# Optimization experiments

Measured on AMD Instinct MI355X. Metric: run time of the kernel, lower is better.

## Reference

```python
import jax, jax.numpy as jnp
import numpy as np

EPS = 1e-3  # kernel epsilon used in Performer generalized kernel
B, H, N, D, M = 1, 8, 1024, 64, 128  # batch, heads, seq, dim_heads, nb_features


def _gaussian_orthogonal_matrix(m, d, seed=0):
    # GaussianOrthogonalRandomMatrix with scaling=0: stacked QR blocks, rows
    # rescaled by chi-distributed norms of gaussian d-vectors.
    rng = np.random.default_rng(seed)
    blocks = []
    for _ in range(m // d):
        g = rng.standard_normal((d, d))
        qmat, _ = np.linalg.qr(g)
        blocks.append(qmat.T)
    proj = np.concatenate(blocks, axis=0)  # [m, d], orthonormal rows per block
    mult = np.linalg.norm(rng.standard_normal((m, d)), axis=1)  # chi norms
    return (mult[:, None] * proj).astype(np.float32)


def setup_inputs() -> dict:
    key = jax.random.key(0)
    kq, kk, kv = jax.random.split(key, 3)
    q = jax.random.normal(kq, (B, H, N, D), dtype=jnp.float32)
    k = jax.random.normal(kk, (B, H, N, D), dtype=jnp.float32)
    v = jax.random.normal(kv, (B, H, N, D), dtype=jnp.float32)
    proj = jnp.asarray(_gaussian_orthogonal_matrix(M, D))
    return {"q": q, "k": k, "v": v, "proj": proj}


def _generalized_kernel(x, proj):
    # kernel_fn(relu)( (x / d**0.25) @ proj^T ) + eps
    normalizer = 1.0 / (x.shape[-1] ** 0.25)
    xp = jnp.einsum('bhnd,md->bhnm', x * normalizer, proj)
    return jax.nn.relu(xp) + EPS


def reference(q, k, v, proj):
    qp = _generalized_kernel(q, proj)  # [B,H,N,M]
    kp = _generalized_kernel(k, proj)  # [B,H,N,M]
    # causal linear attention
    k_cumsum = jnp.cumsum(kp, axis=-2)                              # [B,H,N,M]
    context = jnp.einsum('bhnm,bhne->bhnme', kp, v)                 # [B,H,N,M,D]
    context = jnp.cumsum(context, axis=-3)                          # prefix sums over n
    context = context / k_cumsum[..., None]                         # normalize
    out = jnp.einsum('bhnme,bhnm->bhne', context, qp)               # [B,H,N,D]
    return out
```

## Files before the change

kernel.cpp:

```cpp
#include <hip/hip_runtime.h>

static constexpr int H = 8, N = 1024, D = 64, M = 128, CHUNK = 128, NC = 8;
static constexpr float EPS = 1e-3f;
static constexpr float NORM = 0.35355339059327373f;

typedef __attribute__((ext_vector_type(8))) short short8;
typedef __attribute__((ext_vector_type(4))) float f32x4;

__device__ inline unsigned short f2bf(float x) {
    unsigned u = __float_as_uint(x);
    return (unsigned short)((u + 0x7fffu + ((u >> 16) & 1u)) >> 16);
}
__device__ inline float bf2f(unsigned short u) {
    return __uint_as_float(((unsigned)u) << 16);
}
__device__ inline ushort4 pack4(float4 g) {
    return (ushort4){f2bf(g.x), f2bf(g.y), f2bf(g.z), f2bf(g.w)};
}

__global__ __launch_bounds__(512) void k_projg(const float* __restrict__ q,
                                               const float* __restrict__ k,
                                               const float* __restrict__ proj,
                                               const float* __restrict__ v,
                                               unsigned short* __restrict__ qpb,
                                               unsigned short* __restrict__ kpb,
                                               unsigned short* __restrict__ Gpb,
                                               float* __restrict__ kpart) {
    __shared__ __align__(16) short smem[30208];
    short* projb = smem;
    short* xb = smem + 9216;
    short* obuf = smem + 13824;
    short* kpT = smem + 22528;
    short* vT = smem + 27648;
    const int tid = threadIdx.x;
    const int rblk = blockIdx.x;
    const int h = blockIdx.y;
    const int rowbase = h * N + rblk * 32;
    const int lane = tid & 63, wv = tid >> 6;
    const int rt = wv & 3, mh = wv >> 2;
    const int fr = lane & 15, fq = lane >> 4;

    for (int i4 = tid; i4 < 2048; i4 += 512) {
        int m = i4 >> 4, dq = i4 & 15;
        *(ushort4*)&projb[m * 72 + dq * 4] = pack4(*(const float4*)&proj[i4 * 4]);
    }
    {
        int r = tid >> 4, dq = tid & 15;
        float4 g = *(const float4*)&q[(rowbase + r) * D + dq * 4];
        g.x *= NORM; g.y *= NORM; g.z *= NORM; g.w *= NORM;
        *(ushort4*)&xb[r * 72 + dq * 4] = pack4(g);
        float4 gk = *(const float4*)&k[(rowbase + r) * D + dq * 4];
        gk.x *= NORM; gk.y *= NORM; gk.z *= NORM; gk.w *= NORM;
        *(ushort4*)&xb[(32 + r) * 72 + dq * 4] = pack4(gk);
        int rv = tid & 31, e4 = (tid >> 5) * 4;
        float4 gv = *(const float4*)&v[(rowbase + rv) * D + e4];
        vT[(e4 + 0) * 40 + rv] = (short)f2bf(gv.x);
        vT[(e4 + 1) * 40 + rv] = (short)f2bf(gv.y);
        vT[(e4 + 2) * 40 + rv] = (short)f2bf(gv.z);
        vT[(e4 + 3) * 40 + rv] = (short)f2bf(gv.w);
    }
    __syncthreads();

    f32x4 accp[4];
#pragma unroll
    for (int i = 0; i < 4; i++) accp[i] = (f32x4){0.f, 0.f, 0.f, 0.f};
#pragma unroll
    for (int kt = 0; kt < 2; kt++) {
        short8 a = *(const short8*)&xb[(16 * rt + fr) * 72 + kt * 32 + fq * 8];
#pragma unroll
        for (int i = 0; i < 4; i++) {
            const int mt = mh * 4 + i;
            short8 bb = *(const short8*)&projb[(16 * mt + fr) * 72 + kt * 32 + fq * 8];
            accp[i] = __builtin_amdgcn_mfma_f32_16x16x32_bf16(a, bb, accp[i], 0, 0, 0);
        }
    }
#pragma unroll
    for (int i = 0; i < 4; i++) {
        const int mt = mh * 4 + i;
#pragma unroll
        for (int reg = 0; reg < 4; reg++) {
            const int r = 16 * rt + fq * 4 + reg;
            const int m = 16 * mt + fr;
            unsigned short bv = f2bf(fmaxf(accp[i][reg], 0.f) + EPS);
            obuf[r * 136 + m] = (short)bv;
            if (rt >= 2) kpT[m * 40 + (r - 32)] = (short)bv;
        }
    }
    __syncthreads();

    for (int i = tid; i < 2048; i += 512) {
        int r = i >> 5, cu = i & 31;
        ushort4 val = *(const ushort4*)&obuf[r * 136 + cu * 4];
        unsigned short* g = (r < 32) ? &qpb[(rowbase + r) * M + cu * 4]
                                     : &kpb[(rowbase + r - 32) * M + cu * 4];
        *(ushort4*)g = val;
    }
    const int gb = h * 32 + rblk;
    if (tid < 128) {
        float ks = 0.f;
#pragma unroll 8
        for (int r = 0; r < 32; r++) ks += bf2f((unsigned short)kpT[tid * 40 + r]);
        kpart[gb * M + tid] = ks;
    }
    __syncthreads();

    f32x4 gacc[4];
#pragma unroll
    for (int et = 0; et < 4; et++) gacc[et] = (f32x4){0.f, 0.f, 0.f, 0.f};
    {
        short8 a = *(const short8*)&kpT[(16 * wv + fr) * 40 + fq * 8];
#pragma unroll
        for (int et = 0; et < 4; et++) {
            short8 bb = *(const short8*)&vT[(16 * et + fr) * 40 + fq * 8];
            gacc[et] = __builtin_amdgcn_mfma_f32_16x16x32_bf16(a, bb, gacc[et], 0, 0, 0);
        }
    }
#pragma unroll
    for (int et = 0; et < 4; et++)
#pragma unroll
        for (int reg = 0; reg < 4; reg++) {
            const int m = 16 * wv + fq * 4 + reg;
            obuf[m * 68 + 16 * et + fr] = (short)f2bf(gacc[et][reg]);
        }
    __syncthreads();
    for (int i = tid; i < 2048; i += 512) {
        int m = i >> 4, e4 = (i & 15) * 4;
        *(ushort4*)&Gpb[(gb * M + m) * D + e4] = *(const ushort4*)&obuf[m * 68 + e4];
    }
}

__global__ __launch_bounds__(256) void k_attn(const unsigned short* __restrict__ qpb,
                                              const unsigned short* __restrict__ kpb,
                                              const float* __restrict__ kpart,
                                              const unsigned short* __restrict__ Gpb,
                                              const float* __restrict__ v,
                                              float* __restrict__ out) {
    __shared__ __align__(16) short smem[26112];
    short* bufA = smem;
    short* bufB = smem + 4352;
    short* bufC = smem + 21760;
    short* s0t = bufB;
    short* vT = bufB + 8704;
    const int tid = threadIdx.x;
    const int b = blockIdx.x;
    const int sub = blockIdx.y;
    const int eh = blockIdx.z;
    const int h = b >> 3, c = 7 - (b & 7);
    const int chunkbase = h * N + c * CHUNK;
    const int rowstart = chunkbase + sub * 32;
    const int jrows = (sub + 1) * 32;
    const int lane = tid & 63, wv = tid >> 6;
    const int rt = wv & 1, js = wv >> 1;
    const int fr = lane & 15, fq = lane >> 4;

    {
        const unsigned int* src = (const unsigned int*)kpb;
        for (int i = tid; i < jrows * 64; i += 256) {
            int j = i >> 6, mu = i & 63;
            ((unsigned int*)&bufB[j * 136])[mu] = src[(chunkbase + j) * 64 + mu];
        }
        const unsigned int* srcq = (const unsigned int*)qpb;
        for (int i = tid; i < 2048; i += 256) {
            int r = i >> 6, mu = i & 63;
            ((unsigned int*)&bufC[r * 136])[mu] = srcq[(rowstart + r) * 64 + mu];
        }
    }
    __syncthreads();

    if (tid < 128) {
        const int m = tid;
        float z = 0.f;
        const int send = c * 4 + sub;
        for (int s = 0; s < send; s++) z += kpart[(h * 32 + s) * M + m];
#pragma unroll 8
        for (int r = 0; r < 32; r++) {
            z += bf2f((unsigned short)bufB[(sub * 32 + r) * 136 + m]);
            bufA[r * 136 + m] = (short)f2bf(
                bf2f((unsigned short)bufC[r * 136 + m]) * __builtin_amdgcn_rcpf(z));
        }
    }
    float s0r[16];
#pragma unroll
    for (int j = 0; j < 16; j++) s0r[j] = 0.f;
    {
        const int m = tid >> 1;
        const int ebase = eh * 32 + (tid & 1) * 16;
        for (int cp = 0; cp < c; cp++) {
#pragma unroll
            for (int p = 0; p < 4; p++) {
                const short* gsrc =
                    (const short*)&Gpb[((h * 32 + cp * 4 + p) * M + m) * D + ebase];
                short8 g0 = *(const short8*)&gsrc[0];
                short8 g1 = *(const short8*)&gsrc[8];
#pragma unroll
                for (int j = 0; j < 8; j++) {
                    s0r[j] += bf2f((unsigned short)g0[j]);
                    s0r[8 + j] += bf2f((unsigned short)g1[j]);
                }
            }
        }
    }
    __syncthreads();

    const int jtmax = 2 * sub + 2;
    f32x4 acc1[4];
#pragma unroll
    for (int jl = 0; jl < 4; jl++) acc1[jl] = (f32x4){0.f, 0.f, 0.f, 0.f};
#pragma unroll
    for (int kt = 0; kt < 4; kt++) {
        short8 a = *(const short8*)&bufA[(16 * rt + fr) * 136 + kt * 32 + fq * 8];
#pragma unroll
        for (int jl = 0; jl < 4; jl++) {
            const int jt = js * 4 + jl;
            if (jt < jtmax) {
                short8 bb =
                    *(const short8*)&bufB[(16 * jt + fr) * 136 + kt * 32 + fq * 8];
                acc1[jl] =
                    __builtin_amdgcn_mfma_f32_16x16x32_bf16(a, bb, acc1[jl], 0, 0, 0);
            }
        }
    }
    __syncthreads();

#pragma unroll
    for (int jl = 0; jl < 4; jl++) {
        const int jt = js * 4 + jl;
        if (jt < jtmax) {
            const int j = 16 * jt + fr;
#pragma unroll
            for (int reg = 0; reg < 4; reg++) {
                const int nloc = 16 * rt + fq * 4 + reg;
                float val = (j <= sub * 32 + nloc) ? acc1[jl][reg] : 0.f;
                bufC[nloc * 136 + j] = (short)f2bf(val);
            }
        }
    }
    {
        const int m = tid >> 1;
        const int el = (tid & 1) * 16;
#pragma unroll
        for (int j = 0; j < 16; j++)
            s0t[(el + j) * 136 + m] = (short)f2bf(s0r[j]);
    }
    for (int i = tid; i < jrows * 8; i += 256) {
        int j = i >> 3, e4 = (i & 7) * 4;
        float4 g = *(const float4*)&v[(chunkbase + j) * D + eh * 32 + e4];
        vT[(e4 + 0) * 136 + j] = (short)f2bf(g.x);
        vT[(e4 + 1) * 136 + j] = (short)f2bf(g.y);
        vT[(e4 + 2) * 136 + j] = (short)f2bf(g.z);
        vT[(e4 + 3) * 136 + j] = (short)f2bf(g.w);
    }
    __syncthreads();

    f32x4 acc2 = (f32x4){0.f, 0.f, 0.f, 0.f};
#pragma unroll
    for (int kt = 0; kt < 4; kt++) {
        short8 a = *(const short8*)&bufA[(16 * rt + fr) * 136 + kt * 32 + fq * 8];
        short8 bb = *(const short8*)&s0t[(16 * js + fr) * 136 + kt * 32 + fq * 8];
        acc2 = __builtin_amdgcn_mfma_f32_16x16x32_bf16(a, bb, acc2, 0, 0, 0);
    }
    const int ktmax = sub + 1;
    for (int kt = 0; kt < ktmax; kt++) {
        short8 a = *(const short8*)&bufC[(16 * rt + fr) * 136 + kt * 32 + fq * 8];
        short8 bb = *(const short8*)&vT[(16 * js + fr) * 136 + kt * 32 + fq * 8];
        acc2 = __builtin_amdgcn_mfma_f32_16x16x32_bf16(a, bb, acc2, 0, 0, 0);
    }

#pragma unroll
    for (int reg = 0; reg < 4; reg++) {
        out[(rowstart + 16 * rt + fq * 4 + reg) * D + eh * 32 + 16 * js + fr] =
            acc2[reg];
    }
}

extern "C" void kernel_launch(void* const* d_in, const int* in_sizes, int n_in,
                              void* d_out, int out_size, void* d_ws, size_t ws_size,
                              hipStream_t stream) {
    const float* q = (const float*)d_in[0];
    const float* k = (const float*)d_in[1];
    const float* v = (const float*)d_in[2];
    const float* proj = (const float*)d_in[3];
    float* out = (float*)d_out;

    float* ws = (float*)d_ws;
    float* kpart = ws;
    unsigned short* qpb = (unsigned short*)(kpart + H * 32 * M);
    unsigned short* kpb = qpb + H * N * M;
    unsigned short* Gpb = kpb + H * N * M;

    k_projg<<<dim3(32, H), 512, 0, stream>>>(q, k, proj, v, qpb, kpb, Gpb,
                                             kpart);
    k_attn<<<dim3(H * NC, 4, 2), 256, 0, stream>>>(qpb, kpb, kpart, Gpb, v,
                                                   out);
}
```

Baseline: 91.01 us.

## Fuse projection and attention into one kernel with redundant per-block prefix recompute

Merges the projection/partial-context kernel into the attention kernel. Each block now recomputes the k feature maps, the k-sum prefix and the K^T V prefix for every earlier 32-row group of its head, instead of reading them from workspace. This removes a launch and the global round-trip of qp, kp, G and the k-sum partials. The cost is redundant work: late chunks loop up to 32 groups serially with syncs, which makes per-block work very uneven and adds many MFMA passes over repeated data.

```diff
diff --git a/kernel.cpp b/kernel.cpp
--- a/kernel.cpp
+++ b/kernel.cpp
@@ -18,186 +18,158 @@
     return (ushort4){f2bf(g.x), f2bf(g.y), f2bf(g.z), f2bf(g.w)};
 }
 
-__global__ __launch_bounds__(512) void k_projg(const float* __restrict__ q,
+__global__ __launch_bounds__(256) void k_fused(const float* __restrict__ q,
                                                const float* __restrict__ k,
+                                               const float* __restrict__ v,
                                                const float* __restrict__ proj,
-                                               const float* __restrict__ v,
-                                               unsigned short* __restrict__ qpb,
-                                               unsigned short* __restrict__ kpb,
-                                               unsigned short* __restrict__ Gpb,
-                                               float* __restrict__ kpart) {
-    __shared__ __align__(16) short smem[30208];
-    short* projb = smem;
-    short* xb = smem + 9216;
-    short* obuf = smem + 13824;
-    short* kpT = smem + 22528;
-    short* vT = smem + 27648;
-    const int tid = threadIdx.x;
-    const int rblk = blockIdx.x;
-    const int h = blockIdx.y;
-    const int rowbase = h * N + rblk * 32;
-    const int lane = tid & 63, wv = tid >> 6;
-    const int rt = wv & 3, mh = wv >> 2;
-    const int fr = lane & 15, fq = lane >> 4;
-
-    for (int i4 = tid; i4 < 2048; i4 += 512) {
-        int m = i4 >> 4, dq = i4 & 15;
-        *(ushort4*)&projb[m * 72 + dq * 4] = pack4(*(const float4*)&proj[i4 * 4]);
-    }
-    {
-        int r = tid >> 4, dq = tid & 15;
-        float4 g = *(const float4*)&q[(rowbase + r) * D + dq * 4];
-        g.x *= NORM; g.y *= NORM; g.z *= NORM; g.w *= NORM;
-        *(ushort4*)&xb[r * 72 + dq * 4] = pack4(g);
-        float4 gk = *(const float4*)&k[(rowbase + r) * D + dq * 4];
-        gk.x *= NORM; gk.y *= NORM; gk.z *= NORM; gk.w *= NORM;
-        *(ushort4*)&xb[(32 + r) * 72 + dq * 4] = pack4(gk);
-        int rv = tid & 31, e4 = (tid >> 5) * 4;
-        float4 gv = *(const float4*)&v[(rowbase + rv) * D + e4];
-        vT[(e4 + 0) * 40 + rv] = (short)f2bf(gv.x);
-        vT[(e4 + 1) * 40 + rv] = (short)f2bf(gv.y);
-        vT[(e4 + 2) * 40 + rv] = (short)f2bf(gv.z);
-        vT[(e4 + 3) * 40 + rv] = (short)f2bf(gv.w);
-    }
-    __syncthreads();
-
-    f32x4 accp[4];
-#pragma unroll
-    for (int i = 0; i < 4; i++) accp[i] = (f32x4){0.f, 0.f, 0.f, 0.f};
-#pragma unroll
-    for (int kt = 0; kt < 2; kt++) {
-        short8 a = *(const short8*)&xb[(16 * rt + fr) * 72 + kt * 32 + fq * 8];
-#pragma unroll
-        for (int i = 0; i < 4; i++) {
-            const int mt = mh * 4 + i;
-            short8 bb = *(const short8*)&projb[(16 * mt + fr) * 72 + kt * 32 + fq * 8];
-            accp[i] = __builtin_amdgcn_mfma_f32_16x16x32_bf16(a, bb, accp[i], 0, 0, 0);
-        }
-    }
-#pragma unroll
-    for (int i = 0; i < 4; i++) {
-        const int mt = mh * 4 + i;
-#pragma unroll
-        for (int reg = 0; reg < 4; reg++) {
-            const int r = 16 * rt + fq * 4 + reg;
-            const int m = 16 * mt + fr;
-            unsigned short bv = f2bf(fmaxf(accp[i][reg], 0.f) + EPS);
-            obuf[r * 136 + m] = (short)bv;
-            if (rt >= 2) kpT[m * 40 + (r - 32)] = (short)bv;
-        }
-    }
-    __syncthreads();
-
-    for (int i = tid; i < 2048; i += 512) {
-        int r = i >> 5, cu = i & 31;
-        ushort4 val = *(const ushort4*)&obuf[r * 136 + cu * 4];
-        unsigned short* g = (r < 32) ? &qpb[(rowbase + r) * M + cu * 4]
-                                     : &kpb[(rowbase + r - 32) * M + cu * 4];
-        *(ushort4*)g = val;
-    }
-    const int gb = h * 32 + rblk;
-    if (tid < 128) {
-        float ks = 0.f;
-#pragma unroll 8
-        for (int r = 0; r < 32; r++) ks += bf2f((unsigned short)kpT[tid * 40 + r]);
-        kpart[gb * M + tid] = ks;
-    }
-    __syncthreads();
-
-    f32x4 gacc[4];
-#pragma unroll
-    for (int et = 0; et < 4; et++) gacc[et] = (f32x4){0.f, 0.f, 0.f, 0.f};
-    {
-        short8 a = *(const short8*)&kpT[(16 * wv + fr) * 40 + fq * 8];
-#pragma unroll
-        for (int et = 0; et < 4; et++) {
-            short8 bb = *(const short8*)&vT[(16 * et + fr) * 40 + fq * 8];
-            gacc[et] = __builtin_amdgcn_mfma_f32_16x16x32_bf16(a, bb, gacc[et], 0, 0, 0);
-        }
-    }
-#pragma unroll
-    for (int et = 0; et < 4; et++)
-#pragma unroll
-        for (int reg = 0; reg < 4; reg++) {
-            const int m = 16 * wv + fq * 4 + reg;
-            obuf[m * 68 + 16 * et + fr] = (short)f2bf(gacc[et][reg]);
-        }
-    __syncthreads();
-    for (int i = tid; i < 2048; i += 512) {
-        int m = i >> 4, e4 = (i & 15) * 4;
-        *(ushort4*)&Gpb[(gb * M + m) * D + e4] = *(const ushort4*)&obuf[m * 68 + e4];
-    }
-}
-
-__global__ __launch_bounds__(256) void k_attn(const unsigned short* __restrict__ qpb,
-                                              const unsigned short* __restrict__ kpb,
-                                              const float* __restrict__ kpart,
-                                              const unsigned short* __restrict__ Gpb,
-                                              const float* __restrict__ v,
-                                              float* __restrict__ out) {
-    __shared__ __align__(16) short smem[26112];
-    short* bufA = smem;
-    short* bufB = smem + 4352;
-    short* bufC = smem + 21760;
-    short* s0t = bufB;
-    short* vT = bufB + 8704;
+                                               float* __restrict__ out) {
+    __shared__ __align__(16) short smem[35648];
+    short* bufKp = smem;
+    short* projb = smem + 17408;
+    short* qpl = smem + 17408;
+    short* s0t = smem + 17408;
+    short* Pb = smem + 21760;
+    short* kstage = smem + 26624;
+    short* vT = smem + 28928;
+    short* kpT = smem + 30272;
+    short* W = smem + 30272;
+    short* VT = smem;
+
     const int tid = threadIdx.x;
     const int b = blockIdx.x;
     const int sub = blockIdx.y;
     const int eh = blockIdx.z;
     const int h = b >> 3, c = 7 - (b & 7);
-    const int chunkbase = h * N + c * CHUNK;
-    const int rowstart = chunkbase + sub * 32;
+    const int chunkstart = h * N + c * CHUNK;
+    const int rowstart = chunkstart + sub * 32;
     const int jrows = (sub + 1) * 32;
+    const int gown = c * 4 + sub;
     const int lane = tid & 63, wv = tid >> 6;
     const int rt = wv & 1, js = wv >> 1;
     const int fr = lane & 15, fq = lane >> 4;
 
-    {
-        const unsigned int* src = (const unsigned int*)kpb;
-        for (int i = tid; i < jrows * 64; i += 256) {
-            int j = i >> 6, mu = i & 63;
-            ((unsigned int*)&bufB[j * 136])[mu] = src[(chunkbase + j) * 64 + mu];
-        }
-        const unsigned int* srcq = (const unsigned int*)qpb;
-        for (int i = tid; i < 2048; i += 256) {
-            int r = i >> 6, mu = i & 63;
-            ((unsigned int*)&bufC[r * 136])[mu] = srcq[(rowstart + r) * 64 + mu];
+    for (int i4 = tid; i4 < 2048; i4 += 256) {
+        int m = i4 >> 4, dq = i4 & 15;
+        *(ushort4*)&projb[m * 72 + dq * 4] = pack4(*(const float4*)&proj[i4 * 4]);
+    }
+
+    float zacc = 0.f;
+    f32x4 accG[2][2];
+#pragma unroll
+    for (int i = 0; i < 2; i++)
+#pragma unroll
+        for (int et = 0; et < 2; et++) accG[i][et] = (f32x4){0.f, 0.f, 0.f, 0.f};
+
+    for (int g = 0; g <= gown; ++g) {
+        const int gb = h * N + g * 32;
+        const bool hasv = (g < c * 4);
+        if (g) __syncthreads();
+        for (int i4 = tid; i4 < 512; i4 += 256) {
+            int r = i4 >> 4, dq = i4 & 15;
+            float4 gk = *(const float4*)&k[(gb + r) * D + dq * 4];
+            gk.x *= NORM; gk.y *= NORM; gk.z *= NORM; gk.w *= NORM;
+            *(ushort4*)&kstage[r * 72 + dq * 4] = pack4(gk);
+        }
+        if (hasv) {
+            int r = tid >> 3, e4 = (tid & 7) * 4;
+            float4 gv = *(const float4*)&v[(gb + r) * D + eh * 32 + e4];
+            vT[(e4 + 0) * 42 + r] = (short)f2bf(gv.x);
+            vT[(e4 + 1) * 42 + r] = (short)f2bf(gv.y);
+            vT[(e4 + 2) * 42 + r] = (short)f2bf(gv.z);
+            vT[(e4 + 3) * 42 + r] = (short)f2bf(gv.w);
+        }
+        __syncthreads();
+        f32x4 accp[4];
+#pragma unroll
+        for (int i = 0; i < 4; i++) accp[i] = (f32x4){0.f, 0.f, 0.f, 0.f};
+#pragma unroll
+        for (int kt = 0; kt < 2; kt++) {
+            short8 a = *(const short8*)&kstage[(16 * rt + fr) * 72 + kt * 32 + fq * 8];
+#pragma unroll
+            for (int i = 0; i < 4; i++) {
+                const int mt = js * 4 + i;
+                short8 bb =
+                    *(const short8*)&projb[(16 * mt + fr) * 72 + kt * 32 + fq * 8];
+                accp[i] = __builtin_amdgcn_mfma_f32_16x16x32_bf16(a, bb, accp[i], 0, 0, 0);
+            }
+        }
+        const bool own = (g >= c * 4);
+        const int grow = (g - c * 4) * 32;
+#pragma unroll
+        for (int i = 0; i < 4; i++) {
+            const int mt = js * 4 + i;
+#pragma unroll
+            for (int reg = 0; reg < 4; reg++) {
+                const int r = 16 * rt + fq * 4 + reg;
+                const int m = 16 * mt + fr;
+                unsigned short bv = f2bf(fmaxf(accp[i][reg], 0.f) + EPS);
+                if (g < gown) kpT[m * 42 + r] = (short)bv;
+                if (own) bufKp[(grow + r) * 136 + m] = (short)bv;
+            }
+        }
+        __syncthreads();
+        if (hasv) {
+#pragma unroll
+            for (int i = 0; i < 2; i++) {
+                const int mt = wv * 2 + i;
+                short8 a = *(const short8*)&kpT[(16 * mt + fr) * 42 + fq * 8];
+#pragma unroll
+                for (int et = 0; et < 2; et++) {
+                    short8 bb = *(const short8*)&vT[(16 * et + fr) * 42 + fq * 8];
+                    accG[i][et] =
+                        __builtin_amdgcn_mfma_f32_16x16x32_bf16(a, bb, accG[i][et], 0, 0, 0);
+                }
+            }
+        }
+        if (g < gown && tid < 128) {
+            float ks = 0.f;
+#pragma unroll 8
+            for (int r = 0; r < 32; r++) ks += bf2f((unsigned short)kpT[tid * 42 + r]);
+            zacc += ks;
+        }
+    }
+
+    for (int i4 = tid; i4 < 512; i4 += 256) {
+        int r = i4 >> 4, dq = i4 & 15;
+        float4 gq = *(const float4*)&q[(rowstart + r) * D + dq * 4];
+        gq.x *= NORM; gq.y *= NORM; gq.z *= NORM; gq.w *= NORM;
+        *(ushort4*)&kstage[r * 72 + dq * 4] = pack4(gq);
+    }
+    __syncthreads();
+    f32x4 accq[4];
+#pragma unroll
+    for (int i = 0; i < 4; i++) accq[i] = (f32x4){0.f, 0.f, 0.f, 0.f};
+#pragma unroll
+    for (int kt = 0; kt < 2; kt++) {
+        short8 a = *(const short8*)&kstage[(16 * rt + fr) * 72 + kt * 32 + fq * 8];
+#pragma unroll
+        for (int i = 0; i < 4; i++) {
+            const int mt = js * 4 + i;
+            short8 bb = *(const short8*)&projb[(16 * mt + fr) * 72 + kt * 32 + fq * 8];
+            accq[i] = __builtin_amdgcn_mfma_f32_16x16x32_bf16(a, bb, accq[i], 0, 0, 0);
+        }
+    }
+    __syncthreads();
+#pragma unroll
+    for (int i = 0; i < 4; i++) {
+        const int mt = js * 4 + i;
+#pragma unroll
+        for (int reg = 0; reg < 4; reg++) {
+            const int r = 16 * rt + fq * 4 + reg;
+            const int m = 16 * mt + fr;
+            qpl[r * 136 + m] = (short)f2bf(fmaxf(accq[i][reg], 0.f) + EPS);
         }
     }
     __syncthreads();
 
     if (tid < 128) {
         const int m = tid;
-        float z = 0.f;
-        const int send = c * 4 + sub;
-        for (int s = 0; s < send; s++) z += kpart[(h * 32 + s) * M + m];
+        float z = zacc;
 #pragma unroll 8
         for (int r = 0; r < 32; r++) {
-            z += bf2f((unsigned short)bufB[(sub * 32 + r) * 136 + m]);
-            bufA[r * 136 + m] = (short)f2bf(
-                bf2f((unsigned short)bufC[r * 136 + m]) * __builtin_amdgcn_rcpf(z));
-        }
-    }
-    float s0r[16];
-#pragma unroll
-    for (int j = 0; j < 16; j++) s0r[j] = 0.f;
-    {
-        const int m = tid >> 1;
-        const int ebase = eh * 32 + (tid & 1) * 16;
-        for (int cp = 0; cp < c; cp++) {
-#pragma unroll
-            for (int p = 0; p < 4; p++) {
-                const short* gsrc =
-                    (const short*)&Gpb[((h * 32 + cp * 4 + p) * M + m) * D + ebase];
-                short8 g0 = *(const short8*)&gsrc[0];
-                short8 g1 = *(const short8*)&gsrc[8];
-#pragma unroll
-                for (int j = 0; j < 8; j++) {
-                    s0r[j] += bf2f((unsigned short)g0[j]);
-                    s0r[8 + j] += bf2f((unsigned short)g1[j]);
-                }
-            }
+            z += bf2f((unsigned short)bufKp[(sub * 32 + r) * 136 + m]);
+            W[r * 136 + m] = (short)f2bf(
+                bf2f((unsigned short)qpl[r * 136 + m]) * __builtin_amdgcn_rcpf(z));
         }
     }
     __syncthreads();
@@ -208,13 +180,13 @@
     for (int jl = 0; jl < 4; jl++) acc1[jl] = (f32x4){0.f, 0.f, 0.f, 0.f};
 #pragma unroll
     for (int kt = 0; kt < 4; kt++) {
-        short8 a = *(const short8*)&bufA[(16 * rt + fr) * 136 + kt * 32 + fq * 8];
+        short8 a = *(const short8*)&W[(16 * rt + fr) * 136 + kt * 32 + fq * 8];
 #pragma unroll
         for (int jl = 0; jl < 4; jl++) {
             const int jt = js * 4 + jl;
             if (jt < jtmax) {
                 short8 bb =
-                    *(const short8*)&bufB[(16 * jt + fr) * 136 + kt * 32 + fq * 8];
+                    *(const short8*)&bufKp[(16 * jt + fr) * 136 + kt * 32 + fq * 8];
                 acc1[jl] =
                     __builtin_amdgcn_mfma_f32_16x16x32_bf16(a, bb, acc1[jl], 0, 0, 0);
             }
@@ -231,38 +203,43 @@
             for (int reg = 0; reg < 4; reg++) {
                 const int nloc = 16 * rt + fq * 4 + reg;
                 float val = (j <= sub * 32 + nloc) ? acc1[jl][reg] : 0.f;
-                bufC[nloc * 136 + j] = (short)f2bf(val);
-            }
-        }
-    }
-    {
-        const int m = tid >> 1;
-        const int el = (tid & 1) * 16;
-#pragma unroll
-        for (int j = 0; j < 16; j++)
-            s0t[(el + j) * 136 + m] = (short)f2bf(s0r[j]);
+                Pb[nloc * 136 + j] = (short)f2bf(val);
+            }
+        }
+    }
+#pragma unroll
+    for (int i = 0; i < 2; i++) {
+        const int mt = wv * 2 + i;
+#pragma unroll
+        for (int et = 0; et < 2; et++)
+#pragma unroll
+            for (int reg = 0; reg < 4; reg++) {
+                const int m = 16 * mt + fq * 4 + reg;
+                const int el = 16 * et + fr;
+                s0t[el * 136 + m] = (short)f2bf(accG[i][et][reg]);
+            }
     }
     for (int i = tid; i < jrows * 8; i += 256) {
         int j = i >> 3, e4 = (i & 7) * 4;
-        float4 g = *(const float4*)&v[(chunkbase + j) * D + eh * 32 + e4];
-        vT[(e4 + 0) * 136 + j] = (short)f2bf(g.x);
-        vT[(e4 + 1) * 136 + j] = (short)f2bf(g.y);
-        vT[(e4 + 2) * 136 + j] = (short)f2bf(g.z);
-        vT[(e4 + 3) * 136 + j] = (short)f2bf(g.w);
+        float4 gv = *(const float4*)&v[(chunkstart + j) * D + eh * 32 + e4];
+        VT[(e4 + 0) * 136 + j] = (short)f2bf(gv.x);
+        VT[(e4 + 1) * 136 + j] = (short)f2bf(gv.y);
+        VT[(e4 + 2) * 136 + j] = (short)f2bf(gv.z);
+        VT[(e4 + 3) * 136 + j] = (short)f2bf(gv.w);
     }
     __syncthreads();
 
     f32x4 acc2 = (f32x4){0.f, 0.f, 0.f, 0.f};
 #pragma unroll
     for (int kt = 0; kt < 4; kt++) {
-        short8 a = *(const short8*)&bufA[(16 * rt + fr) * 136 + kt * 32 + fq * 8];
+        short8 a = *(const short8*)&W[(16 * rt + fr) * 136 + kt * 32 + fq * 8];
         short8 bb = *(const short8*)&s0t[(16 * js + fr) * 136 + kt * 32 + fq * 8];
         acc2 = __builtin_amdgcn_mfma_f32_16x16x32_bf16(a, bb, acc2, 0, 0, 0);
     }
     const int ktmax = sub + 1;
     for (int kt = 0; kt < ktmax; kt++) {
-        short8 a = *(const short8*)&bufC[(16 * rt + fr) * 136 + kt * 32 + fq * 8];
-        short8 bb = *(const short8*)&vT[(16 * js + fr) * 136 + kt * 32 + fq * 8];
+        short8 a = *(const short8*)&Pb[(16 * rt + fr) * 136 + kt * 32 + fq * 8];
+        short8 bb = *(const short8*)&VT[(16 * js + fr) * 136 + kt * 32 + fq * 8];
         acc2 = __builtin_amdgcn_mfma_f32_16x16x32_bf16(a, bb, acc2, 0, 0, 0);
     }
 
@@ -281,15 +258,7 @@
     const float* v = (const float*)d_in[2];
     const float* proj = (const float*)d_in[3];
     float* out = (float*)d_out;
-
-    float* ws = (float*)d_ws;
-    float* kpart = ws;
-    unsigned short* qpb = (unsigned short*)(kpart + H * 32 * M);
-    unsigned short* kpb = qpb + H * N * M;
-    unsigned short* Gpb = kpb + H * N * M;
-
-    k_projg<<<dim3(32, H), 512, 0, stream>>>(q, k, proj, v, qpb, kpb, Gpb,
-                                             kpart);
-    k_attn<<<dim3(H * NC, 4, 2), 256, 0, stream>>>(qpb, kpb, kpart, Gpb, v,
-                                                   out);
-}
+    (void)d_ws; (void)ws_size;
+
+    k_fused<<<dim3(H * NC, 4, 2), 256, 0, stream>>>(q, k, v, proj, out);
+}
```

Result: slower. 166.2 us (+82.6%).
